# Kernel tuning notes

Hardware: AMD Instinct MI355X
Metric: run time of the kernel (lower is better)

## Reference

```python
import jax, jax.numpy as jnp
import numpy as np


def setup_inputs() -> dict:
    key = jax.random.key(0)
    k1, k2, k3 = jax.random.split(key, 3)
    B, N, T_BG, T_IN = 32, 64, 512, 256
    surv_steps = jax.random.uniform(k1, (B, N, T_BG), dtype=jnp.float32)
    time_bg = jax.random.uniform(k2, (T_BG,), dtype=jnp.float32)
    time_in = jax.random.uniform(k3, (T_IN,), dtype=jnp.float32)
    bandwidth = jnp.ones((1,), dtype=jnp.float32)  # learned parameter
    return {
        "surv_steps": surv_steps,
        "time_bg": time_bg,
        "time_in": time_in,
        "bandwidth": bandwidth,
        "single_time": 0,
    }


def reference(surv_steps, time_bg, time_in, bandwidth, single_time):
    # bandwidth.clamp_min(1e-6)
    b = jnp.maximum(bandwidth, 1e-6)  # [1]
    # pairwise abs time difference: [T_in, T_bg]
    t_metric = jnp.abs(time_bg[None, :] - time_in[:, None])
    # softmin(x) == softmax(-x), over the background-time axis
    t_weights = jax.nn.softmax(-(b * t_metric), axis=-1)  # [T_in, T_bg]
    if single_time:
        # t_weights -> [T_in, 1, T_bg], surv_hist = surv_steps broadcast over middle dim
        proba = jnp.sum(t_weights[:, None, :] * surv_steps, axis=-1)
    else:
        # t_weights -> [1,1,T_in,T_bg], surv_hist = surv_steps[..., None, :]
        # sum over T_bg == contraction: [B,N,T_bg] x [T_in,T_bg] -> [B,N,T_in]
        proba = jnp.einsum("bnt,it->bni", surv_steps, t_weights)
    return proba
```

## Files before the change

kernel.cpp:

```cpp
#include <hip/hip_runtime.h>
#include <math.h>

constexpr int TBG = 512;
constexpr int TIN = 256;
constexpr int M   = 2048;

constexpr int BM = 64, BN = 64, BK = 32;
constexpr int KSPLIT = 4;
constexpr int KC  = TBG / KSPLIT;
constexpr int LDK = BK + 4;

__global__ __launch_bounds__(256, 2) void fused_kernel(
    const float* __restrict__ A,
    const float* __restrict__ time_bg,
    const float* __restrict__ time_in,
    const float* __restrict__ bandwidth,
    float* __restrict__ C)
{
    __shared__ float tbg_s[TBG];
    __shared__ float As[BM][LDK];
    __shared__ float Es[BN][LDK];
    __shared__ float red[BN][4];
    __shared__ float invS[BN];

    const int tid = threadIdx.x;
    const int i0  = blockIdx.x * BN;
    const int m0  = blockIdx.y * BM;
    const int kk0 = blockIdx.z * KC;

    const float b = fmaxf(bandwidth[0], 1e-6f);

    tbg_s[tid]       = time_bg[tid];
    tbg_s[tid + 256] = time_bg[tid + 256];
    __syncthreads();

    {
        const int   i  = tid >> 2;
        const int   q  = tid & 3;
        const float ti = time_in[i0 + i];
        float s = 0.f;
        #pragma unroll 4
        for (int j = 0; j < 128; ++j)
            s += __expf(-b * fabsf(tbg_s[q * 128 + j] - ti));
        red[i][q] = s;
    }
    __syncthreads();
    if (tid < BN)
        invS[tid] = 1.0f / (red[tid][0] + red[tid][1] + red[tid][2] + red[tid][3]);

    const int   ar   = tid >> 2;
    const int   ac   = (tid & 3) << 3;
    const float ti_e = time_in[i0 + ar];

    const int tx = tid & 15;
    const int ty = tid >> 4;

    float acc[4][4] = {};

    for (int k0 = 0; k0 < KC; k0 += BK) {
        const int kk = kk0 + k0;

        const float4 a4a = *(const float4*)(A + (m0 + ar) * TBG + kk + ac);
        const float4 a4b = *(const float4*)(A + (m0 + ar) * TBG + kk + ac + 4);

        float e[8];
        #pragma unroll
        for (int j = 0; j < 8; ++j)
            e[j] = __expf(-b * fabsf(tbg_s[kk + ac + j] - ti_e));

        *(float4*)&As[ar][ac]     = a4a;
        *(float4*)&As[ar][ac + 4] = a4b;
        *(float4*)&Es[ar][ac]     = make_float4(e[0], e[1], e[2], e[3]);
        *(float4*)&Es[ar][ac + 4] = make_float4(e[4], e[5], e[6], e[7]);
        __syncthreads();

        #pragma unroll
        for (int k4 = 0; k4 < BK / 4; ++k4) {
            float4 av[4], ev[4];
            #pragma unroll
            for (int r = 0; r < 4; ++r)
                av[r] = *(const float4*)&As[ty + 16 * r][k4 * 4];
            #pragma unroll
            for (int c = 0; c < 4; ++c)
                ev[c] = *(const float4*)&Es[tx + 16 * c][k4 * 4];
            #pragma unroll
            for (int r = 0; r < 4; ++r)
                #pragma unroll
                for (int c = 0; c < 4; ++c)
                    acc[r][c] += av[r].x * ev[c].x + av[r].y * ev[c].y
                               + av[r].z * ev[c].z + av[r].w * ev[c].w;
        }
        __syncthreads();
    }

    float is[4];
    #pragma unroll
    for (int c = 0; c < 4; ++c)
        is[c] = invS[tx + 16 * c];
    #pragma unroll
    for (int r = 0; r < 4; ++r)
        #pragma unroll
        for (int c = 0; c < 4; ++c)
            unsafeAtomicAdd(&C[(m0 + ty + 16 * r) * TIN + i0 + tx + 16 * c],
                            acc[r][c] * is[c]);
}

extern "C" void kernel_launch(void* const* d_in, const int* in_sizes, int n_in,
                              void* d_out, int out_size, void* d_ws, size_t ws_size,
                              hipStream_t stream)
{
    const float* surv      = (const float*)d_in[0];
    const float* time_bg   = (const float*)d_in[1];
    const float* time_in   = (const float*)d_in[2];
    const float* bandwidth = (const float*)d_in[3];

    float* out = (float*)d_out;

    hipMemsetAsync(out, 0, (size_t)out_size * sizeof(float), stream);

    fused_kernel<<<dim3(TIN / BN, M / BM, KSPLIT), dim3(256), 0, stream>>>(
        surv, time_bg, time_in, bandwidth, out);
}
```

Measured before the change: 81.53 us.

## Switch to bf16 MFMA GEMM with factored exp weights and no split-K

Replaces the FP32 SIMT split-K GEMM with bf16 MFMA 16x16x32 instructions, converting both the input tile and the softmax weight matrix to bf16 in shared memory. The weight tile is precomputed once per block using a factored form exp(-b|x-y|) = min(e^{bx}e^{-by}, e^{-bx}e^{by}), which replaces per-element exp with multiplies. It drops split-K, the atomics and the memset for direct stores. This cuts FP32 FMA work and launch overhead, at the cost of bf16 precision loss and possible overflow in the factored exponentials for large b*t.

```diff
diff --git a/kernel.cpp b/kernel.cpp
--- a/kernel.cpp
+++ b/kernel.cpp
@@ -5,104 +5,131 @@
 constexpr int TIN = 256;
 constexpr int M   = 2048;
 
-constexpr int BM = 64, BN = 64, BK = 32;
-constexpr int KSPLIT = 4;
-constexpr int KC  = TBG / KSPLIT;
-constexpr int LDK = BK + 4;
+constexpr int BM = 32;
+constexpr int BN = 64;
+constexpr int BK = 128;
+constexpr int EPAD = 8;
+constexpr int APAD = 8;
 
-__global__ __launch_bounds__(256, 2) void fused_kernel(
+typedef __attribute__((ext_vector_type(8))) short bf16x8;
+typedef __attribute__((ext_vector_type(4))) float f32x4;
+
+__device__ __forceinline__ unsigned short f2bf(float f) {
+    unsigned u = __float_as_uint(f);
+    u += 0x7FFFu + ((u >> 16) & 1u);
+    return (unsigned short)(u >> 16);
+}
+
+__global__ __launch_bounds__(512, 2) void fused_kernel(
     const float* __restrict__ A,
     const float* __restrict__ time_bg,
     const float* __restrict__ time_in,
     const float* __restrict__ bandwidth,
     float* __restrict__ C)
 {
-    __shared__ float tbg_s[TBG];
-    __shared__ float As[BM][LDK];
-    __shared__ float Es[BN][LDK];
-    __shared__ float red[BN][4];
+    __shared__ unsigned short Es[BN][TBG + EPAD];
+    __shared__ unsigned short As[BM][BK + APAD];
+    __shared__ float Pt[TBG];
+    __shared__ float Pti[TBG];
+    __shared__ float red[BN][8];
     __shared__ float invS[BN];
 
     const int tid = threadIdx.x;
     const int i0  = blockIdx.x * BN;
     const int m0  = blockIdx.y * BM;
-    const int kk0 = blockIdx.z * KC;
-
     const float b = fmaxf(bandwidth[0], 1e-6f);
 
-    tbg_s[tid]       = time_bg[tid];
-    tbg_s[tid + 256] = time_bg[tid + 256];
+    {
+        const float t = time_bg[tid];
+        Pt[tid]  = __expf(b * t);
+        Pti[tid] = __expf(-b * t);
+    }
     __syncthreads();
 
     {
-        const int   i  = tid >> 2;
-        const int   q  = tid & 3;
-        const float ti = time_in[i0 + i];
+        const int   i   = tid >> 3;
+        const int   o   = tid & 7;
+        const float ti  = time_in[i0 + i];
+        const float qi  = __expf(-b * ti);
+        const float qii = __expf(b * ti);
         float s = 0.f;
-        #pragma unroll 4
-        for (int j = 0; j < 128; ++j)
-            s += __expf(-b * fabsf(tbg_s[q * 128 + j] - ti));
-        red[i][q] = s;
+        #pragma unroll
+        for (int j0 = 0; j0 < 64; j0 += 8) {
+            const int t0 = o * 64 + j0;
+            const float4 p0  = *(const float4*)&Pt[t0];
+            const float4 p1  = *(const float4*)&Pt[t0 + 4];
+            const float4 q0  = *(const float4*)&Pti[t0];
+            const float4 q1  = *(const float4*)&Pti[t0 + 4];
+            float e[8];
+            e[0] = fminf(p0.x * qi, q0.x * qii);
+            e[1] = fminf(p0.y * qi, q0.y * qii);
+            e[2] = fminf(p0.z * qi, q0.z * qii);
+            e[3] = fminf(p0.w * qi, q0.w * qii);
+            e[4] = fminf(p1.x * qi, q1.x * qii);
+            e[5] = fminf(p1.y * qi, q1.y * qii);
+            e[6] = fminf(p1.z * qi, q1.z * qii);
+            e[7] = fminf(p1.w * qi, q1.w * qii);
+            bf16x8 pk;
+            #pragma unroll
+            for (int j = 0; j < 8; ++j) {
+                s += e[j];
+                pk[j] = (short)f2bf(e[j]);
+            }
+            *(bf16x8*)&Es[i][t0] = pk;
+        }
+        red[i][o] = s;
     }
     __syncthreads();
-    if (tid < BN)
-        invS[tid] = 1.0f / (red[tid][0] + red[tid][1] + red[tid][2] + red[tid][3]);
 
-    const int   ar   = tid >> 2;
-    const int   ac   = (tid & 3) << 3;
-    const float ti_e = time_in[i0 + ar];
+    if (tid < BN) {
+        float s = 0.f;
+        #pragma unroll
+        for (int o = 0; o < 8; ++o) s += red[tid][o];
+        invS[tid] = 1.0f / s;
+    }
 
-    const int tx = tid & 15;
-    const int ty = tid >> 4;
+    const int w    = tid >> 6;
+    const int mt   = w >> 2;
+    const int ig   = w & 3;
+    const int lane = tid & 63;
+    const int col  = lane & 15;
+    const int quad = lane >> 4;
 
-    float acc[4][4] = {};
+    const int ar = tid >> 4;
+    const int ac = (tid & 15) << 3;
 
-    for (int k0 = 0; k0 < KC; k0 += BK) {
-        const int kk = kk0 + k0;
+    f32x4 acc = {0.f, 0.f, 0.f, 0.f};
 
-        const float4 a4a = *(const float4*)(A + (m0 + ar) * TBG + kk + ac);
-        const float4 a4b = *(const float4*)(A + (m0 + ar) * TBG + kk + ac + 4);
-
-        float e[8];
-        #pragma unroll
-        for (int j = 0; j < 8; ++j)
-            e[j] = __expf(-b * fabsf(tbg_s[kk + ac + j] - ti_e));
-
-        *(float4*)&As[ar][ac]     = a4a;
-        *(float4*)&As[ar][ac + 4] = a4b;
-        *(float4*)&Es[ar][ac]     = make_float4(e[0], e[1], e[2], e[3]);
-        *(float4*)&Es[ar][ac + 4] = make_float4(e[4], e[5], e[6], e[7]);
+    for (int k0 = 0; k0 < TBG; k0 += BK) {
+        {
+            const float* ap = A + (m0 + ar) * TBG + k0 + ac;
+            const float4 x = *(const float4*)ap;
+            const float4 y = *(const float4*)(ap + 4);
+            bf16x8 pk;
+            pk[0] = (short)f2bf(x.x); pk[1] = (short)f2bf(x.y);
+            pk[2] = (short)f2bf(x.z); pk[3] = (short)f2bf(x.w);
+            pk[4] = (short)f2bf(y.x); pk[5] = (short)f2bf(y.y);
+            pk[6] = (short)f2bf(y.z); pk[7] = (short)f2bf(y.w);
+            *(bf16x8*)&As[ar][ac] = pk;
+        }
         __syncthreads();
 
         #pragma unroll
-        for (int k4 = 0; k4 < BK / 4; ++k4) {
-            float4 av[4], ev[4];
-            #pragma unroll
-            for (int r = 0; r < 4; ++r)
-                av[r] = *(const float4*)&As[ty + 16 * r][k4 * 4];
-            #pragma unroll
-            for (int c = 0; c < 4; ++c)
-                ev[c] = *(const float4*)&Es[tx + 16 * c][k4 * 4];
-            #pragma unroll
-            for (int r = 0; r < 4; ++r)
-                #pragma unroll
-                for (int c = 0; c < 4; ++c)
-                    acc[r][c] += av[r].x * ev[c].x + av[r].y * ev[c].y
-                               + av[r].z * ev[c].z + av[r].w * ev[c].w;
+        for (int s = 0; s < 4; ++s) {
+            const int ks = s * 32 + quad * 8;
+            const bf16x8 bfr = *(const bf16x8*)&Es[ig * 16 + col][k0 + ks];
+            const bf16x8 afr = *(const bf16x8*)&As[mt * 16 + col][ks];
+            acc = __builtin_amdgcn_mfma_f32_16x16x32_bf16(afr, bfr, acc, 0, 0, 0);
         }
         __syncthreads();
     }
 
-    float is[4];
+    const float isv = invS[ig * 16 + col];
     #pragma unroll
-    for (int c = 0; c < 4; ++c)
-        is[c] = invS[tx + 16 * c];
-    #pragma unroll
-    for (int r = 0; r < 4; ++r)
-        #pragma unroll
-        for (int c = 0; c < 4; ++c)
-            unsafeAtomicAdd(&C[(m0 + ty + 16 * r) * TIN + i0 + tx + 16 * c],
-                            acc[r][c] * is[c]);
+    for (int v = 0; v < 4; ++v) {
+        const int m = m0 + mt * 16 + quad * 4 + v;
+        C[m * TIN + i0 + ig * 16 + col] = acc[v] * isv;
+    }
 }
 
 extern "C" void kernel_launch(void* const* d_in, const int* in_sizes, int n_in,
@@ -116,8 +143,6 @@
 
     float* out = (float*)d_out;
 
-    hipMemsetAsync(out, 0, (size_t)out_size * sizeof(float), stream);
-
-    fused_kernel<<<dim3(TIN / BN, M / BM, KSPLIT), dim3(256), 0, stream>>>(
+    fused_kernel<<<dim3(TIN / BN, M / BM), dim3(512), 0, stream>>>(
         surv, time_bg, time_in, bandwidth, out);
 }
```

Result: faster. 70.63 us (-13.4%).
